# Kernel optimization log

Measured on AMD Instinct MI355X. Metric: run time of the kernel, lower is better.

## Reference

```python
import jax, jax.numpy as jnp
import numpy as np

TEMP = 16.0  # sqrt(in_dim=256), module default when temperature=None
BN_EPS = 1e-5


def setup_inputs() -> dict:
    key = jax.random.key(0)
    ks = jax.random.split(key, 8)
    B, Cin, T, H, W = 8, 256, 8, 16, 16
    FF, Cout = 512, 256
    # small init scale keeps softmax logits in a sane range
    s = 0.02
    return {
        "x": jax.random.normal(ks[0], (B, Cin, T, H, W), jnp.float32),
        "Wk": jax.random.normal(ks[1], (FF, Cin), jnp.float32) * s,
        "Wq": jax.random.normal(ks[2], (FF, Cin), jnp.float32) * s,
        "Wv": jax.random.normal(ks[3], (FF, Cin), jnp.float32) * s,
        "Wout": jax.random.normal(ks[4], (Cout, FF), jnp.float32) * s,
        "bout": jax.random.normal(ks[5], (Cout,), jnp.float32) * s,
        "gamma": jnp.ones((Cout,), jnp.float32),
        "beta": jnp.zeros((Cout,), jnp.float32),
    }


def reference(x, Wk, Wq, Wv, Wout, bout, gamma, beta):
    B, Cin, T, H, W = x.shape
    N = T * H * W
    xf = x.reshape(B, Cin, N)                      # 1x1x1 conv == per-position matmul
    K = jnp.einsum('fc,bcn->bfn', Wk, xf)
    Q = jnp.einsum('fc,bcn->bfn', Wq, xf)
    V = jnp.einsum('fc,bcn->bfn', Wv, xf)
    KQ = jnp.einsum('bfi,bfj->bij', K, Q)          # [B, N, N] = K^T Q
    attn = jax.nn.softmax(KQ / TEMP, axis=2)
    # torch: sum(V[:, :, :, None] * attn[:, None], dim=3)
    #      = V[b,c,i] * sum_j attn[b,i,j]  (no need to materialize B x C x N x N)
    agg = V * jnp.sum(attn, axis=2)[:, None, :]    # [B, FF, N]
    o = jnp.einsum('of,bfn->bon', Wout, agg) + bout[None, :, None]
    o = jax.nn.relu(o).reshape(B, -1, T, H, W)
    y = x + o                                      # residual (in_dim == out_dim)
    # BatchNorm3d, training mode (fresh module): batch stats over (B, T, H, W)
    mean = jnp.mean(y, axis=(0, 2, 3, 4), keepdims=True)
    var = jnp.var(y, axis=(0, 2, 3, 4), keepdims=True)
    g = gamma[None, :, None, None, None]
    b = beta[None, :, None, None, None]
    return g * (y - mean) * jax.lax.rsqrt(var + BN_EPS) + b
```

## Files before the change

kernel.cpp:

```cpp
#include <hip/hip_runtime.h>

typedef __attribute__((ext_vector_type(8))) short short8;
typedef __attribute__((ext_vector_type(4))) float floatx4;

#define CIN  256
#define NSP  2048
#define COUT 256

__device__ __forceinline__ unsigned short f2bf_rne(float f) {
  unsigned int u = __float_as_uint(f);
  u += 0x7fffu + ((u >> 16) & 1u);
  return (unsigned short)(u >> 16);
}

__device__ __forceinline__ unsigned int pack_bf16_hu(float lo, float hi) {
  unsigned int a = __float_as_uint(lo) + 0x8000u;
  unsigned int b = __float_as_uint(hi) + 0x8000u;
  return __builtin_amdgcn_perm(b, a, 0x07060302u);
}

__global__ __launch_bounds__(1024) void k1_m(
    const float* __restrict__ Wv, const float* __restrict__ Wout,
    unsigned short* __restrict__ Mb, float* __restrict__ stats)
{
  __shared__ float ws[512];
  __shared__ float red[4][256];
  const int tid = threadIdx.x;
  const int r   = blockIdx.x;
  if (r == 0 && tid < 512) stats[tid] = 0.f;
  if (tid < 512) ws[tid] = Wout[(size_t)r * 512 + tid];
  __syncthreads();
  const int c  = tid & 255;
  const int fs = tid >> 8;
  float acc = 0.f;
  #pragma unroll 16
  for (int f0 = 0; f0 < 128; ++f0) {
    int f = fs * 128 + f0;
    acc += ws[f] * Wv[(size_t)f * 256 + c];
  }
  red[fs][c] = acc;
  __syncthreads();
  if (tid < 256) {
    float s = red[0][tid] + red[1][tid] + red[2][tid] + red[3][tid];
    Mb[(size_t)r * 256 + tid] = f2bf_rne(s);
  }
}

__global__ __launch_bounds__(256) void k2_gemm(
    const float* __restrict__ x, const unsigned short* __restrict__ Mb,
    const float* __restrict__ bout, float* __restrict__ stats,
    float* __restrict__ out)
{
  __shared__ float ls[128], lq[128];
  const int tid  = threadIdx.x;
  const int lane = tid & 63;
  const int wave = tid >> 6;
  const int m16  = lane & 15;
  const int q    = lane >> 4;
  const int nb   = blockIdx.x * 64;
  const int ocb  = blockIdx.y * 128;
  const int b    = blockIdx.z;
  const int wocb = ocb + (wave & 1) * 64;
  const int wnb  = nb + (wave >> 1) * 32;

  if (tid < 128) { ls[tid] = 0.f; lq[tid] = 0.f; }

  floatx4 acc[4][2];
  #pragma unroll
  for (int i = 0; i < 4; ++i)
    #pragma unroll
    for (int j = 0; j < 2; ++j)
      acc[i][j] = (floatx4){0.f, 0.f, 0.f, 0.f};

  const unsigned short* Ab = Mb + (size_t)(wocb + m16) * 256 + q * 8;
  const float* xb = x + (size_t)b * CIN * NSP;
  const float* Bb = xb + (size_t)(q * 8) * NSP + wnb + m16;

  #pragma unroll
  for (int kk = 0; kk < 8; ++kk) {
    short8 av[4];
    #pragma unroll
    for (int ti = 0; ti < 4; ++ti)
      av[ti] = *(const short8*)(Ab + (size_t)ti * 16 * 256 + kk * 32);
    short8 bv[2];
    #pragma unroll
    for (int tj = 0; tj < 2; ++tj) {
      const float* bp = Bb + (size_t)(kk * 32) * NSP + tj * 16;
      union { unsigned int u[4]; short8 v; } p;
      #pragma unroll
      for (int j = 0; j < 4; ++j) {
        float f0 = bp[(size_t)(2 * j) * NSP];
        float f1 = bp[(size_t)(2 * j + 1) * NSP];
        p.u[j] = pack_bf16_hu(f0, f1);
      }
      bv[tj] = p.v;
    }
    #pragma unroll
    for (int ti = 0; ti < 4; ++ti)
      #pragma unroll
      for (int tj = 0; tj < 2; ++tj)
        acc[ti][tj] = __builtin_amdgcn_mfma_f32_16x16x32_bf16(av[ti], bv[tj], acc[ti][tj], 0, 0, 0);
  }

  __syncthreads();

  #pragma unroll
  for (int ti = 0; ti < 4; ++ti) {
    #pragma unroll
    for (int r = 0; r < 4; ++r) {
      const int ocl = (wave & 1) * 64 + ti * 16 + q * 4 + r;
      const int oc  = ocb + ocl;
      const float bo = bout[oc];
      float s = 0.f, s2 = 0.f;
      #pragma unroll
      for (int tj = 0; tj < 2; ++tj) {
        const int n = wnb + tj * 16 + m16;
        const size_t gidx = ((size_t)(b * COUT + oc)) * NSP + n;
        float o = fmaxf(acc[ti][tj][r] + bo, 0.f);
        float y = x[gidx] + o;
        out[gidx] = y;
        s += y;
        s2 += y * y;
      }
      #pragma unroll
      for (int d = 1; d < 16; d <<= 1) {
        s  += __shfl_xor(s, d, 64);
        s2 += __shfl_xor(s2, d, 64);
      }
      if (m16 == 0) {
        atomicAdd(&ls[ocl], s);
        atomicAdd(&lq[ocl], s2);
      }
    }
  }
  __syncthreads();
  if (tid < 128) {
    atomicAdd(&stats[ocb + tid], ls[tid]);
    atomicAdd(&stats[256 + ocb + tid], lq[tid]);
  }
}

__global__ __launch_bounds__(256) void k3_norm(
    const float* __restrict__ stats, const float* __restrict__ gamma,
    const float* __restrict__ beta, float* __restrict__ out)
{
  const int row = blockIdx.x;
  const int oc  = row & 255;
  const float inv_n = 1.f / 16384.f;
  const float m  = stats[oc] * inv_n;
  const float v  = stats[256 + oc] * inv_n - m * m;
  const float sc = gamma[oc] * rsqrtf(v + 1e-5f);
  const float sh = beta[oc] - m * sc;
  float* p = out + (size_t)row * 2048 + threadIdx.x * 8;
  float4 a = *(const float4*)p;
  float4 c = *(const float4*)(p + 4);
  a.x = a.x * sc + sh; a.y = a.y * sc + sh;
  a.z = a.z * sc + sh; a.w = a.w * sc + sh;
  c.x = c.x * sc + sh; c.y = c.y * sc + sh;
  c.z = c.z * sc + sh; c.w = c.w * sc + sh;
  *(float4*)p = a;
  *(float4*)(p + 4) = c;
}

extern "C" void kernel_launch(void* const* d_in, const int* in_sizes, int n_in,
                              void* d_out, int out_size, void* d_ws, size_t ws_size,
                              hipStream_t stream) {
  const float* x     = (const float*)d_in[0];
  const float* Wv    = (const float*)d_in[3];
  const float* Wout  = (const float*)d_in[4];
  const float* bout  = (const float*)d_in[5];
  const float* gamma = (const float*)d_in[6];
  const float* beta  = (const float*)d_in[7];
  float* out = (float*)d_out;

  char* w = (char*)d_ws;
  unsigned short* Mb = (unsigned short*)w;
  float* stats = (float*)(w + 131072);

  hipLaunchKernelGGL(k1_m,    dim3(256),       dim3(1024), 0, stream,
                     Wv, Wout, Mb, stats);
  hipLaunchKernelGGL(k2_gemm, dim3(32, 2, 8),  dim3(256),  0, stream,
                     x, Mb, bout, stats, out);
  hipLaunchKernelGGL(k3_norm, dim3(2048),      dim3(256),  0, stream,
                     stats, gamma, beta, out);
}
```

Baseline: 114.0 us.

## Fuse BatchNorm into GEMM via grid-wide barrier, keeping results in registers

The separate normalization kernel is removed. The GEMM kernel now keeps the residual sums in accumulator registers and publishes per-channel statistics. It then waits on a global atomic counter until all 256 blocks arrive, and applies scale and shift before one final store to the output. This removes a full extra read-modify-write pass over the output and one kernel launch. It also hoists all x loads ahead of the MFMA loop and reworks k1 to compute 4 rows per block. The spin barrier relies on all blocks being co-resident, which the grid size (256 blocks, launch bounds of 2 per CU) is meant to guarantee. If they are not co-resident, it risks deadlock.

```diff
diff --git a/kernel.cpp b/kernel.cpp
--- a/kernel.cpp
+++ b/kernel.cpp
@@ -19,37 +19,34 @@
   return __builtin_amdgcn_perm(b, a, 0x07060302u);
 }
 
-__global__ __launch_bounds__(1024) void k1_m(
+__global__ __launch_bounds__(256) void k1_m(
     const float* __restrict__ Wv, const float* __restrict__ Wout,
-    unsigned short* __restrict__ Mb, float* __restrict__ stats)
+    unsigned short* __restrict__ Mb)
 {
-  __shared__ float ws[512];
-  __shared__ float red[4][256];
+  __shared__ float ws[4 * 512];
   const int tid = threadIdx.x;
-  const int r   = blockIdx.x;
-  if (r == 0 && tid < 512) stats[tid] = 0.f;
-  if (tid < 512) ws[tid] = Wout[(size_t)r * 512 + tid];
-  __syncthreads();
-  const int c  = tid & 255;
-  const int fs = tid >> 8;
-  float acc = 0.f;
-  #pragma unroll 16
-  for (int f0 = 0; f0 < 128; ++f0) {
-    int f = fs * 128 + f0;
-    acc += ws[f] * Wv[(size_t)f * 256 + c];
-  }
-  red[fs][c] = acc;
-  __syncthreads();
-  if (tid < 256) {
-    float s = red[0][tid] + red[1][tid] + red[2][tid] + red[3][tid];
-    Mb[(size_t)r * 256 + tid] = f2bf_rne(s);
-  }
-}
-
-__global__ __launch_bounds__(256) void k2_gemm(
+  const int rbase = blockIdx.x * 4;
+  #pragma unroll
+  for (int i = 0; i < 8; ++i)
+    ws[i * 256 + tid] = Wout[(size_t)rbase * 512 + i * 256 + tid];
+  __syncthreads();
+  float a4[4] = {0.f, 0.f, 0.f, 0.f};
+  #pragma unroll 8
+  for (int f = 0; f < 512; ++f) {
+    float w = Wv[(size_t)f * 256 + tid];
+    #pragma unroll
+    for (int j = 0; j < 4; ++j) a4[j] += ws[j * 512 + f] * w;
+  }
+  #pragma unroll
+  for (int j = 0; j < 4; ++j)
+    Mb[(size_t)(rbase + j) * 256 + tid] = f2bf_rne(a4[j]);
+}
+
+__global__ __launch_bounds__(512, 2) void k2_fused(
     const float* __restrict__ x, const unsigned short* __restrict__ Mb,
-    const float* __restrict__ bout, float* __restrict__ stats,
-    float* __restrict__ out)
+    const float* __restrict__ bout, const float* __restrict__ gamma,
+    const float* __restrict__ beta, float* __restrict__ stats,
+    int* __restrict__ scount, float* __restrict__ out)
 {
   __shared__ float ls[128], lq[128];
   const int tid  = threadIdx.x;
@@ -57,7 +54,7 @@
   const int wave = tid >> 6;
   const int m16  = lane & 15;
   const int q    = lane >> 4;
-  const int nb   = blockIdx.x * 64;
+  const int nb   = blockIdx.x * 128;
   const int ocb  = blockIdx.y * 128;
   const int b    = blockIdx.z;
   const int wocb = ocb + (wave & 1) * 64;
@@ -65,24 +62,10 @@
 
   if (tid < 128) { ls[tid] = 0.f; lq[tid] = 0.f; }
 
-  floatx4 acc[4][2];
-  #pragma unroll
-  for (int i = 0; i < 4; ++i)
-    #pragma unroll
-    for (int j = 0; j < 2; ++j)
-      acc[i][j] = (floatx4){0.f, 0.f, 0.f, 0.f};
-
-  const unsigned short* Ab = Mb + (size_t)(wocb + m16) * 256 + q * 8;
-  const float* xb = x + (size_t)b * CIN * NSP;
-  const float* Bb = xb + (size_t)(q * 8) * NSP + wnb + m16;
-
+  const float* Bb = x + (size_t)b * CIN * NSP + (size_t)(q * 8) * NSP + wnb + m16;
+  short8 bv[8][2];
   #pragma unroll
   for (int kk = 0; kk < 8; ++kk) {
-    short8 av[4];
-    #pragma unroll
-    for (int ti = 0; ti < 4; ++ti)
-      av[ti] = *(const short8*)(Ab + (size_t)ti * 16 * 256 + kk * 32);
-    short8 bv[2];
     #pragma unroll
     for (int tj = 0; tj < 2; ++tj) {
       const float* bp = Bb + (size_t)(kk * 32) * NSP + tj * 16;
@@ -93,13 +76,29 @@
         float f1 = bp[(size_t)(2 * j + 1) * NSP];
         p.u[j] = pack_bf16_hu(f0, f1);
       }
-      bv[tj] = p.v;
+      bv[kk][tj] = p.v;
     }
+  }
+
+  floatx4 acc[4][2];
+  #pragma unroll
+  for (int i = 0; i < 4; ++i)
+    #pragma unroll
+    for (int j = 0; j < 2; ++j)
+      acc[i][j] = (floatx4){0.f, 0.f, 0.f, 0.f};
+
+  const unsigned short* Ab = Mb + (size_t)(wocb + m16) * 256 + q * 8;
+  #pragma unroll
+  for (int kk = 0; kk < 8; ++kk) {
+    short8 av[4];
     #pragma unroll
     for (int ti = 0; ti < 4; ++ti)
+      av[ti] = *(const short8*)(Ab + (size_t)ti * 16 * 256 + kk * 32);
+    #pragma unroll
+    for (int ti = 0; ti < 4; ++ti)
       #pragma unroll
       for (int tj = 0; tj < 2; ++tj)
-        acc[ti][tj] = __builtin_amdgcn_mfma_f32_16x16x32_bf16(av[ti], bv[tj], acc[ti][tj], 0, 0, 0);
+        acc[ti][tj] = __builtin_amdgcn_mfma_f32_16x16x32_bf16(av[ti], bv[kk][tj], acc[ti][tj], 0, 0, 0);
   }
 
   __syncthreads();
@@ -118,7 +117,7 @@
         const size_t gidx = ((size_t)(b * COUT + oc)) * NSP + n;
         float o = fmaxf(acc[ti][tj][r] + bo, 0.f);
         float y = x[gidx] + o;
-        out[gidx] = y;
+        acc[ti][tj][r] = y;
         s += y;
         s2 += y * y;
       }
@@ -138,28 +137,45 @@
     atomicAdd(&stats[ocb + tid], ls[tid]);
     atomicAdd(&stats[256 + ocb + tid], lq[tid]);
   }
-}
-
-__global__ __launch_bounds__(256) void k3_norm(
-    const float* __restrict__ stats, const float* __restrict__ gamma,
-    const float* __restrict__ beta, float* __restrict__ out)
-{
-  const int row = blockIdx.x;
-  const int oc  = row & 255;
-  const float inv_n = 1.f / 16384.f;
-  const float m  = stats[oc] * inv_n;
-  const float v  = stats[256 + oc] * inv_n - m * m;
-  const float sc = gamma[oc] * rsqrtf(v + 1e-5f);
-  const float sh = beta[oc] - m * sc;
-  float* p = out + (size_t)row * 2048 + threadIdx.x * 8;
-  float4 a = *(const float4*)p;
-  float4 c = *(const float4*)(p + 4);
-  a.x = a.x * sc + sh; a.y = a.y * sc + sh;
-  a.z = a.z * sc + sh; a.w = a.w * sc + sh;
-  c.x = c.x * sc + sh; c.y = c.y * sc + sh;
-  c.z = c.z * sc + sh; c.w = c.w * sc + sh;
-  *(float4*)p = a;
-  *(float4*)(p + 4) = c;
+
+  __threadfence();
+  __syncthreads();
+  if (tid == 0) {
+    __hip_atomic_fetch_add(scount, 1, __ATOMIC_ACQ_REL, __HIP_MEMORY_SCOPE_AGENT);
+    while (__hip_atomic_load(scount, __ATOMIC_ACQUIRE, __HIP_MEMORY_SCOPE_AGENT) < 256)
+      __builtin_amdgcn_s_sleep(2);
+  }
+  __syncthreads();
+
+  if (tid < 128) {
+    const int oc = ocb + tid;
+    const float inv_n = 1.f / 16384.f;
+    float sm = __hip_atomic_load(&stats[oc], __ATOMIC_RELAXED, __HIP_MEMORY_SCOPE_AGENT);
+    float sq = __hip_atomic_load(&stats[256 + oc], __ATOMIC_RELAXED, __HIP_MEMORY_SCOPE_AGENT);
+    float m = sm * inv_n;
+    float v = sq * inv_n - m * m;
+    float sc = gamma[oc] * rsqrtf(v + 1e-5f);
+    ls[tid] = sc;
+    lq[tid] = beta[oc] - m * sc;
+  }
+  __syncthreads();
+
+  #pragma unroll
+  for (int ti = 0; ti < 4; ++ti) {
+    #pragma unroll
+    for (int r = 0; r < 4; ++r) {
+      const int ocl = (wave & 1) * 64 + ti * 16 + q * 4 + r;
+      const int oc  = ocb + ocl;
+      const float sc = ls[ocl];
+      const float sh = lq[ocl];
+      #pragma unroll
+      for (int tj = 0; tj < 2; ++tj) {
+        const int n = wnb + tj * 16 + m16;
+        const size_t gidx = ((size_t)(b * COUT + oc)) * NSP + n;
+        out[gidx] = acc[ti][tj][r] * sc + sh;
+      }
+    }
+  }
 }
 
 extern "C" void kernel_launch(void* const* d_in, const int* in_sizes, int n_in,
@@ -176,11 +192,11 @@
   char* w = (char*)d_ws;
   unsigned short* Mb = (unsigned short*)w;
   float* stats = (float*)(w + 131072);
-
-  hipLaunchKernelGGL(k1_m,    dim3(256),       dim3(1024), 0, stream,
-                     Wv, Wout, Mb, stats);
-  hipLaunchKernelGGL(k2_gemm, dim3(32, 2, 8),  dim3(256),  0, stream,
-                     x, Mb, bout, stats, out);
-  hipLaunchKernelGGL(k3_norm, dim3(2048),      dim3(256),  0, stream,
-                     stats, gamma, beta, out);
-}
+  int* scount  = (int*)(w + 131072 + 2048);
+
+  hipMemsetAsync(stats, 0, 4096, stream);
+
+  hipLaunchKernelGGL(k1_m, dim3(64), dim3(256), 0, stream, Wv, Wout, Mb);
+  hipLaunchKernelGGL(k2_fused, dim3(16, 2, 8), dim3(512), 0, stream,
+                     x, Mb, bout, gamma, beta, stats, scount, out);
+}
```

After: 161.9 us. 42.0% more time.

## Store pre-norm activations as bf16 and rebalance weight-fold and GEMM tiling

Applied to the files above, without the earlier changes.

The GEMM kernel now writes the residual sum y as bf16 into a workspace buffer, and the normalization kernel reads it back and writes fp32 output, halving intermediate traffic. The weight-fold kernel computes four output rows per block, so Wv is re-read a quarter as often. GEMM tiles shrink to 32 columns with twice as many blocks and an occupancy hint. The trade-off is that bf16 rounding of y adds error to the final normalized output.

```diff
diff --git a/kernel.cpp b/kernel.cpp
--- a/kernel.cpp
+++ b/kernel.cpp
@@ -19,37 +19,34 @@
   return __builtin_amdgcn_perm(b, a, 0x07060302u);
 }
 
-__global__ __launch_bounds__(1024) void k1_m(
+__global__ __launch_bounds__(256) void k1_m(
     const float* __restrict__ Wv, const float* __restrict__ Wout,
     unsigned short* __restrict__ Mb, float* __restrict__ stats)
 {
-  __shared__ float ws[512];
-  __shared__ float red[4][256];
+  __shared__ float ws[4 * 512];
   const int tid = threadIdx.x;
-  const int r   = blockIdx.x;
-  if (r == 0 && tid < 512) stats[tid] = 0.f;
-  if (tid < 512) ws[tid] = Wout[(size_t)r * 512 + tid];
+  const int rbase = blockIdx.x * 4;
+  if (blockIdx.x == 0) { stats[tid] = 0.f; stats[256 + tid] = 0.f; }
+  #pragma unroll
+  for (int i = 0; i < 8; ++i)
+    ws[i * 256 + tid] = Wout[(size_t)rbase * 512 + i * 256 + tid];
   __syncthreads();
-  const int c  = tid & 255;
-  const int fs = tid >> 8;
-  float acc = 0.f;
-  #pragma unroll 16
-  for (int f0 = 0; f0 < 128; ++f0) {
-    int f = fs * 128 + f0;
-    acc += ws[f] * Wv[(size_t)f * 256 + c];
+  float a4[4] = {0.f, 0.f, 0.f, 0.f};
+  #pragma unroll 8
+  for (int f = 0; f < 512; ++f) {
+    float w = Wv[(size_t)f * 256 + tid];
+    #pragma unroll
+    for (int j = 0; j < 4; ++j) a4[j] += ws[j * 512 + f] * w;
   }
-  red[fs][c] = acc;
-  __syncthreads();
-  if (tid < 256) {
-    float s = red[0][tid] + red[1][tid] + red[2][tid] + red[3][tid];
-    Mb[(size_t)r * 256 + tid] = f2bf_rne(s);
-  }
+  #pragma unroll
+  for (int j = 0; j < 4; ++j)
+    Mb[(size_t)(rbase + j) * 256 + tid] = f2bf_rne(a4[j]);
 }
 
-__global__ __launch_bounds__(256) void k2_gemm(
+__global__ __launch_bounds__(256, 4) void k2_gemm(
     const float* __restrict__ x, const unsigned short* __restrict__ Mb,
     const float* __restrict__ bout, float* __restrict__ stats,
-    float* __restrict__ out)
+    unsigned short* __restrict__ ybf)
 {
   __shared__ float ls[128], lq[128];
   const int tid  = threadIdx.x;
@@ -57,71 +54,52 @@
   const int wave = tid >> 6;
   const int m16  = lane & 15;
   const int q    = lane >> 4;
-  const int nb   = blockIdx.x * 64;
+  const int nb   = blockIdx.x * 32;
   const int ocb  = blockIdx.y * 128;
   const int b    = blockIdx.z;
   const int wocb = ocb + (wave & 1) * 64;
-  const int wnb  = nb + (wave >> 1) * 32;
+  const int wn   = nb + (wave >> 1) * 16;
 
   if (tid < 128) { ls[tid] = 0.f; lq[tid] = 0.f; }
 
-  floatx4 acc[4][2];
+  floatx4 acc[4];
   #pragma unroll
-  for (int i = 0; i < 4; ++i)
-    #pragma unroll
-    for (int j = 0; j < 2; ++j)
-      acc[i][j] = (floatx4){0.f, 0.f, 0.f, 0.f};
+  for (int i = 0; i < 4; ++i) acc[i] = (floatx4){0.f, 0.f, 0.f, 0.f};
 
   const unsigned short* Ab = Mb + (size_t)(wocb + m16) * 256 + q * 8;
-  const float* xb = x + (size_t)b * CIN * NSP;
-  const float* Bb = xb + (size_t)(q * 8) * NSP + wnb + m16;
+  const float* Bb = x + (size_t)b * CIN * NSP + (size_t)(q * 8) * NSP + wn + m16;
 
   #pragma unroll
   for (int kk = 0; kk < 8; ++kk) {
-    short8 av[4];
+    const float* bp = Bb + (size_t)(kk * 32) * NSP;
+    union { unsigned int u[4]; short8 v; } p;
     #pragma unroll
-    for (int ti = 0; ti < 4; ++ti)
-      av[ti] = *(const short8*)(Ab + (size_t)ti * 16 * 256 + kk * 32);
-    short8 bv[2];
-    #pragma unroll
-    for (int tj = 0; tj < 2; ++tj) {
-      const float* bp = Bb + (size_t)(kk * 32) * NSP + tj * 16;
-      union { unsigned int u[4]; short8 v; } p;
-      #pragma unroll
-      for (int j = 0; j < 4; ++j) {
-        float f0 = bp[(size_t)(2 * j) * NSP];
-        float f1 = bp[(size_t)(2 * j + 1) * NSP];
-        p.u[j] = pack_bf16_hu(f0, f1);
-      }
-      bv[tj] = p.v;
+    for (int j = 0; j < 4; ++j) {
+      float f0 = bp[(size_t)(2 * j) * NSP];
+      float f1 = bp[(size_t)(2 * j + 1) * NSP];
+      p.u[j] = pack_bf16_hu(f0, f1);
     }
     #pragma unroll
-    for (int ti = 0; ti < 4; ++ti)
-      #pragma unroll
-      for (int tj = 0; tj < 2; ++tj)
-        acc[ti][tj] = __builtin_amdgcn_mfma_f32_16x16x32_bf16(av[ti], bv[tj], acc[ti][tj], 0, 0, 0);
+    for (int ti = 0; ti < 4; ++ti) {
+      short8 av = *(const short8*)(Ab + (size_t)ti * 16 * 256 + kk * 32);
+      acc[ti] = __builtin_amdgcn_mfma_f32_16x16x32_bf16(av, p.v, acc[ti], 0, 0, 0);
+    }
   }
 
   __syncthreads();
 
+  const int n = wn + m16;
   #pragma unroll
   for (int ti = 0; ti < 4; ++ti) {
     #pragma unroll
     for (int r = 0; r < 4; ++r) {
       const int ocl = (wave & 1) * 64 + ti * 16 + q * 4 + r;
       const int oc  = ocb + ocl;
-      const float bo = bout[oc];
-      float s = 0.f, s2 = 0.f;
-      #pragma unroll
-      for (int tj = 0; tj < 2; ++tj) {
-        const int n = wnb + tj * 16 + m16;
-        const size_t gidx = ((size_t)(b * COUT + oc)) * NSP + n;
-        float o = fmaxf(acc[ti][tj][r] + bo, 0.f);
-        float y = x[gidx] + o;
-        out[gidx] = y;
-        s += y;
-        s2 += y * y;
-      }
+      const size_t gidx = ((size_t)(b * COUT + oc)) * NSP + n;
+      float o = fmaxf(acc[ti][r] + bout[oc], 0.f);
+      float y = x[gidx] + o;
+      ybf[gidx] = f2bf_rne(y);
+      float s = y, s2 = y * y;
       #pragma unroll
       for (int d = 1; d < 16; d <<= 1) {
         s  += __shfl_xor(s, d, 64);
@@ -142,7 +120,8 @@
 
 __global__ __launch_bounds__(256) void k3_norm(
     const float* __restrict__ stats, const float* __restrict__ gamma,
-    const float* __restrict__ beta, float* __restrict__ out)
+    const float* __restrict__ beta, const unsigned short* __restrict__ ybf,
+    float* __restrict__ out)
 {
   const int row = blockIdx.x;
   const int oc  = row & 255;
@@ -151,15 +130,19 @@
   const float v  = stats[256 + oc] * inv_n - m * m;
   const float sc = gamma[oc] * rsqrtf(v + 1e-5f);
   const float sh = beta[oc] - m * sc;
-  float* p = out + (size_t)row * 2048 + threadIdx.x * 8;
-  float4 a = *(const float4*)p;
-  float4 c = *(const float4*)(p + 4);
-  a.x = a.x * sc + sh; a.y = a.y * sc + sh;
-  a.z = a.z * sc + sh; a.w = a.w * sc + sh;
-  c.x = c.x * sc + sh; c.y = c.y * sc + sh;
-  c.z = c.z * sc + sh; c.w = c.w * sc + sh;
-  *(float4*)p = a;
-  *(float4*)(p + 4) = c;
+  const size_t base = (size_t)row * 2048 + threadIdx.x * 8;
+  const uint4 raw = *(const uint4*)(ybf + base);
+  float4 o0, o1;
+  o0.x = __uint_as_float(raw.x << 16)         * sc + sh;
+  o0.y = __uint_as_float(raw.x & 0xffff0000u) * sc + sh;
+  o0.z = __uint_as_float(raw.y << 16)         * sc + sh;
+  o0.w = __uint_as_float(raw.y & 0xffff0000u) * sc + sh;
+  o1.x = __uint_as_float(raw.z << 16)         * sc + sh;
+  o1.y = __uint_as_float(raw.z & 0xffff0000u) * sc + sh;
+  o1.z = __uint_as_float(raw.w << 16)         * sc + sh;
+  o1.w = __uint_as_float(raw.w & 0xffff0000u) * sc + sh;
+  *(float4*)(out + base)     = o0;
+  *(float4*)(out + base + 4) = o1;
 }
 
 extern "C" void kernel_launch(void* const* d_in, const int* in_sizes, int n_in,
@@ -176,11 +159,12 @@
   char* w = (char*)d_ws;
   unsigned short* Mb = (unsigned short*)w;
   float* stats = (float*)(w + 131072);
+  unsigned short* ybf = (unsigned short*)(w + 131072 + 4096);
 
-  hipLaunchKernelGGL(k1_m,    dim3(256),       dim3(1024), 0, stream,
+  hipLaunchKernelGGL(k1_m,    dim3(64),        dim3(256), 0, stream,
                      Wv, Wout, Mb, stats);
-  hipLaunchKernelGGL(k2_gemm, dim3(32, 2, 8),  dim3(256),  0, stream,
-                     x, Mb, bout, stats, out);
-  hipLaunchKernelGGL(k3_norm, dim3(2048),      dim3(256),  0, stream,
-                     stats, gamma, beta, out);
+  hipLaunchKernelGGL(k2_gemm, dim3(64, 2, 8),  dim3(256), 0, stream,
+                     x, Mb, bout, stats, ybf);
+  hipLaunchKernelGGL(k3_norm, dim3(2048),      dim3(256), 0, stream,
+                     stats, gamma, beta, ybf, out);
 }
```

After: 139.9 us. 1.23x slower.
